# Optimization experiments

Measured on AMD Instinct MI355X. Metric: run time of the kernel, lower is better.

Reference implementation:

```python
import jax, jax.numpy as jnp
import numpy as np

N_NODES = 100000
N_EDGES = 1600000
N_REL = 8
N_HEADS = 4
IN_FEAT = 128
OUT_FEAT = 64
D_HEAD = OUT_FEAT // N_HEADS
LEAKY_SLOPE = 0.2


def setup_inputs() -> dict:
    key = jax.random.key(0)
    ks = jax.random.split(key, 8)
    inputs = jax.random.normal(ks[0], (N_NODES, IN_FEAT), dtype=jnp.float32)
    conv_weights = jax.random.normal(ks[1], (N_REL, N_HEADS, IN_FEAT, D_HEAD), dtype=jnp.float32) * (1.0 / np.sqrt(IN_FEAT))
    attn_l = jax.random.normal(ks[2], (N_REL, N_HEADS, D_HEAD), dtype=jnp.float32) * (1.0 / np.sqrt(D_HEAD))
    attn_r = jax.random.normal(ks[3], (N_REL, N_HEADS, D_HEAD), dtype=jnp.float32) * (1.0 / np.sqrt(D_HEAD))
    h_bias = jax.random.normal(ks[4], (OUT_FEAT,), dtype=jnp.float32)
    src_idx = jax.random.randint(ks[5], (N_EDGES,), 0, N_NODES, dtype=jnp.int64) if jax.config.jax_enable_x64 else jax.random.randint(ks[5], (N_EDGES,), 0, N_NODES, dtype=jnp.int32)
    dst_idx = jax.random.randint(ks[6], (N_EDGES,), 0, N_NODES, dtype=src_idx.dtype)
    rel_idx = jax.random.randint(ks[7], (N_EDGES,), 0, N_REL, dtype=src_idx.dtype)
    return {"inputs": inputs, "conv_weights": conv_weights, "attn_l": attn_l,
            "attn_r": attn_r, "h_bias": h_bias, "src_idx": src_idx,
            "dst_idx": dst_idx, "rel_idx": rel_idx}


def reference(inputs, conv_weights, attn_l, attn_r, h_bias, src_idx, dst_idx, rel_idx):
    N = inputs.shape[0]
    # Per-node per-relation projection: [N, R, H, Dh]
    # (equivalent math to the per-relation grouped matmul over unique nodes)
    proj = jnp.einsum('ni,rhid->nrhd', inputs, conv_weights)
    # Gather per-edge src/dst projected features under the edge's relation: [E, H, Dh]
    feat_src = proj[src_idx, rel_idx]
    feat_dst = proj[dst_idx, rel_idx]
    # Attention logits per edge/head: [E, H]
    el = jnp.sum(feat_src * attn_l[rel_idx], axis=-1)
    er = jnp.sum(feat_dst * attn_r[rel_idx], axis=-1)
    score = jax.nn.leaky_relu(el + er, negative_slope=LEAKY_SLOPE)
    # Edge softmax over incoming edges of each destination node (per head)
    smax = jax.ops.segment_max(score, dst_idx, num_segments=N)        # [N, H]
    e = jnp.exp(score - smax[dst_idx])                                # [E, H]
    denom = jax.ops.segment_sum(e, dst_idx, num_segments=N)          # [N, H]
    alpha = e / denom[dst_idx]                                        # [E, H]
    # Weighted aggregation of src features to dst nodes: [N, H, Dh]
    h = jax.ops.segment_sum(alpha[..., None] * feat_src, dst_idx, num_segments=N)
    h = h.reshape(N, OUT_FEAT) + h_bias
    return h
```

## Files before the change

kernel.cpp:

```cpp
#include <hip/hip_runtime.h>
#include <hip/hip_bf16.h>


#define NN 100000
#define NNP 100096
#define NE 1600000
#define NH 4
#define INF_ 128
#define DH 16
#define NCOL 576
#define LEAKY 0.2f
#define NBUCK 391
#define BSHIFT 8
#define CHUNK 4096
#define CAP 5120
#define WEXT_BLOCKS 288

typedef __hip_bfloat16 bf16;
typedef __attribute__((ext_vector_type(8))) short bf16x8;
typedef __attribute__((ext_vector_type(4))) short bf16x4;
typedef __attribute__((ext_vector_type(4))) float f32x4;

static __device__ __forceinline__ short f2bs(float x) {
    bf16 b = __float2bfloat16(x);
    return *reinterpret_cast<short*>(&b);
}
static __device__ __forceinline__ float bflo(unsigned u) { return __uint_as_float(u << 16); }
static __device__ __forceinline__ float bfhi(unsigned u) { return __uint_as_float(u & 0xffff0000u); }

__global__ __launch_bounds__(256) void wext_scatter(
    const float* __restrict__ W, const float* __restrict__ al, const float* __restrict__ ar,
    short* __restrict__ wxt2,
    const int* __restrict__ src, const int* __restrict__ dst, const int* __restrict__ rel,
    int* __restrict__ gCursor, int* __restrict__ pairbuf) {
    __shared__ int hist[NBUCK];
    int t = threadIdx.x;

    if (blockIdx.x >= WEXT_BLOCKS) {
        int blk = blockIdx.x - WEXT_BLOCKS;
        for (int i = t; i < NBUCK; i += 256) hist[i] = 0;
        __syncthreads();
        int base = blk * CHUNK;
        #pragma unroll
        for (int j = 0; j < CHUNK / 256; ++j) {
            int e = base + j * 256 + t;
            if (e < NE) atomicAdd(&hist[dst[e] >> BSHIFT], 1);
        }
        __syncthreads();
        for (int i = t; i < NBUCK; i += 256) {
            int v = hist[i];
            hist[i] = v ? (i * CAP + atomicAdd(&gCursor[i], v)) : 0;
        }
        __syncthreads();
        #pragma unroll
        for (int j = 0; j < CHUNK / 256; ++j) {
            int e = base + j * 256 + t;
            if (e < NE) {
                int d = dst[e];
                int b = d >> BSHIFT;
                int rec = ((d & 255) << 20) | (src[e] * 8 + rel[e]);
                int pos = atomicAdd(&hist[b], 1);
                pairbuf[pos] = rec;
            }
        }
        return;
    }

    int idx = blockIdx.x * 256 + t;
    int e = idx & 7, lane = (idx >> 3) & 63, ct = (idx >> 9) & 3, ks = (idx >> 11) & 3, cb = idx >> 13;
    int g = lane >> 4, r = lane & 15;
    int c = cb * 64 + ct * 16 + r;
    int k = ks * 32 + g * 8 + e;
    float v;
    if (c < 512) {
        int rr = c >> 6, rem = c & 63, h = rem >> 4, d = rem & 15;
        v = W[((rr * NH + h) * INF_ + k) * DH + d];
    } else {
        int rh = c - 512;
        const float* a = al;
        if (rh >= 32) { rh -= 32; a = ar; }
        int rr = rh >> 2, h = rh & 3;
        const float* wp = &W[((rr * NH + h) * INF_ + k) * DH];
        const float* ap = &a[(rr * NH + h) * DH];
        float s = 0.f;
        #pragma unroll
        for (int d = 0; d < DH; ++d) s += wp[d] * ap[d];
        v = s;
    }
    wxt2[idx] = f2bs(v);
}

__global__ __launch_bounds__(256) void gemm_direct(
    const float* __restrict__ A, const short* __restrict__ WxT2,
    bf16* __restrict__ projR, float* __restrict__ elr) {
    __shared__ short As[16384];
    __shared__ short Bs[8192];
    int t = threadIdx.x;
    int wv = t >> 6, lane = t & 63;
    int n0 = blockIdx.x * 128;
    int g = lane >> 4, r = lane & 15;

    #pragma unroll
    for (int j = 0; j < 8; ++j) {
        int i = j * 256 + t;
        int row = i >> 4, c8 = i & 15;
        int gr = n0 + row;
        bf16x8 v;
        if (gr < NN) {
            float4 f0 = *(const float4*)&A[gr * INF_ + c8 * 8];
            float4 f1 = *(const float4*)&A[gr * INF_ + c8 * 8 + 4];
            v[0] = f2bs(f0.x); v[1] = f2bs(f0.y); v[2] = f2bs(f0.z); v[3] = f2bs(f0.w);
            v[4] = f2bs(f1.x); v[5] = f2bs(f1.y); v[6] = f2bs(f1.z); v[7] = f2bs(f1.w);
        } else {
            v = (bf16x8)(short)0;
        }
        *(bf16x8*)&As[(row * 16 + (c8 ^ (row & 7))) * 8] = v;
    }
    bf16x8 breg[4];
    #pragma unroll
    for (int q = 0; q < 4; ++q)
        breg[q] = *(const bf16x8*)&WxT2[(q * 256 + t) * 8];
    __syncthreads();

    bf16x8 afr[2][4];
    #pragma unroll
    for (int nt = 0; nt < 2; ++nt) {
        int row = wv * 32 + nt * 16 + r;
        #pragma unroll
        for (int ks = 0; ks < 4; ++ks)
            afr[nt][ks] = *(const bf16x8*)&As[(row * 16 + ((ks * 4 + g) ^ (r & 7))) * 8];
    }
    __syncthreads();
    short* Csh = &As[wv * 4096];
    float* Csf = (float*)Csh;
    int n0w = n0 + wv * 32;

    for (int cb = 0; cb < 9; ++cb) {
        #pragma unroll
        for (int q = 0; q < 4; ++q)
            *(bf16x8*)&Bs[(q * 256 + t) * 8] = breg[q];
        __syncthreads();
        if (cb < 8) {
            #pragma unroll
            for (int q = 0; q < 4; ++q)
                breg[q] = *(const bf16x8*)&WxT2[((cb + 1) * 1024 + q * 256 + t) * 8];
        }

        f32x4 acc[2][4] = {};
        #pragma unroll
        for (int ks = 0; ks < 4; ++ks) {
            #pragma unroll
            for (int ct = 0; ct < 4; ++ct) {
                bf16x8 b = *(const bf16x8*)&Bs[((ks * 4 + ct) * 64 + lane) * 8];
                acc[0][ct] = __builtin_amdgcn_mfma_f32_16x16x32_bf16(b, afr[0][ks], acc[0][ct], 0, 0, 0);
                acc[1][ct] = __builtin_amdgcn_mfma_f32_16x16x32_bf16(b, afr[1][ks], acc[1][ct], 0, 0, 0);
            }
        }
        if (cb < 8) {
            #pragma unroll
            for (int nt = 0; nt < 2; ++nt) {
                int rr = nt * 16 + r;
                #pragma unroll
                for (int ct = 0; ct < 4; ++ct) {
                    bf16x4 p;
                    p[0] = f2bs(acc[nt][ct][0]); p[1] = f2bs(acc[nt][ct][1]);
                    p[2] = f2bs(acc[nt][ct][2]); p[3] = f2bs(acc[nt][ct][3]);
                    *(bf16x4*)&Csh[rr * 64 + (((ct * 4 + g) ^ ((rr & 7) << 1)) << 2)] = p;
                }
            }
            __builtin_amdgcn_wave_barrier();
            size_t base = ((size_t)cb * NN + n0w) * 64;
            #pragma unroll
            for (int q = 0; q < 4; ++q) {
                int rr = (lane >> 3) + q * 8;
                if (n0w + rr < NN) {
                    bf16x8 vv = *(const bf16x8*)&Csh[rr * 64 + (((lane & 7) ^ (rr & 7)) << 3)];
                    __builtin_nontemporal_store(vv, (bf16x8*)&((short*)projR)[base + q * 512 + lane * 8]);
                }
            }
            __builtin_amdgcn_wave_barrier();
        } else {
            #pragma unroll
            for (int nt = 0; nt < 2; ++nt) {
                int rr = nt * 16 + r;
                #pragma unroll
                for (int ct = 0; ct < 4; ++ct)
                    *(f32x4*)&Csf[rr * 64 + (((ct * 4 + g) ^ ((rr & 7) << 1)) << 2)] = acc[nt][ct];
            }
            __builtin_amdgcn_wave_barrier();
            #pragma unroll
            for (int q = 0; q < 8; ++q) {
                int rr = (lane >> 4) + q * 4;
                if (n0w + rr < NN) {
                    f32x4 vv = *(const f32x4*)&Csf[rr * 64 + (((lane & 15) ^ ((rr & 7) << 1)) << 2)];
                    __builtin_nontemporal_store(vv, (f32x4*)&elr[(size_t)n0w * 64 + q * 256 + lane * 4]);
                }
            }
        }
        __syncthreads();
    }
}

__global__ __launch_bounds__(256) void exact_place(
    const int* __restrict__ gCursor, const int* __restrict__ pairbuf,
    int2* __restrict__ offdeg, int2* __restrict__ rec2) {
    __shared__ int hist[256];
    __shared__ int tsum[256];
    int b = blockIdx.x, t = threadIdx.x;
    int start = b * CAP, cnt = gCursor[b];
    hist[t] = 0;
    __syncthreads();
    for (int i = t; i < cnt; i += 256) atomicAdd(&hist[pairbuf[start + i] >> 20], 1);
    __syncthreads();
    int own = hist[t];
    tsum[t] = own;
    __syncthreads();
    for (int st = 1; st < 256; st <<= 1) {
        int y = (t >= st) ? tsum[t - st] : 0;
        __syncthreads();
        tsum[t] += y;
        __syncthreads();
    }
    int excl = start + tsum[t] - own;
    int node = b * 256 + t;
    if (node < NN) offdeg[node] = make_int2(excl, own);
    __syncthreads();
    hist[t] = excl;
    __syncthreads();
    for (int i = t; i < cnt; i += 256) {
        int rec = pairbuf[start + i];
        int pos = atomicAdd(&hist[rec >> 20], 1);
        int sr = rec & 0xFFFFF;
        rec2[pos] = make_int2((sr >> 3) * 64 + (sr & 7) * 4,
                              (sr & 7) * (NN * 64) + (sr >> 3) * 64);
    }
}

__global__ __launch_bounds__(256) void agg(
    const int2* __restrict__ offdeg, const int2* __restrict__ rec2,
    const float* __restrict__ elr, const bf16* __restrict__ projR,
    const float* __restrict__ bias, float* __restrict__ out) {
    __shared__ float s_alpha[4][64][4];
    __shared__ int   s_pidx[4][64];
    __shared__ float s_er[4][32];
    int wv = threadIdx.x >> 6, lane = threadIdx.x & 63;
    int d = blockIdx.x * 4 + wv;
    if (d >= NN) return;
    int2 od = offdeg[d];
    int off = od.x, deg = od.y;
    int end = off + deg;

    if (lane < 32) s_er[wv][lane] = elr[d * 64 + 32 + lane];
    __builtin_amdgcn_wave_barrier();
    asm volatile("s_waitcnt lgkmcnt(0)" ::: "memory");

    if (deg == 0) {
        if (lane < 32) {
            float2 bb = *(const float2*)&bias[lane * 2];
            *(float2*)&out[d * 64 + lane * 2] = bb;
        }
    } else if (deg <= 64) {
        int i = off + lane;
        float e0 = 0.f, e1 = 0.f, e2 = 0.f, e3 = 0.f;
        int pidx = 0;
        if (i < end) {
            int2 rv = rec2[i];
            pidx = rv.y;
            float4 el4 = *(const float4*)&elr[rv.x];
            int erb = rv.x & 63;
            float x;
            x = el4.x + s_er[wv][erb + 0]; x = x > 0.f ? x : LEAKY * x; e0 = __expf(x);
            x = el4.y + s_er[wv][erb + 1]; x = x > 0.f ? x : LEAKY * x; e1 = __expf(x);
            x = el4.z + s_er[wv][erb + 2]; x = x > 0.f ? x : LEAKY * x; e2 = __expf(x);
            x = el4.w + s_er[wv][erb + 3]; x = x > 0.f ? x : LEAKY * x; e3 = __expf(x);
        }
        s_pidx[wv][lane] = pidx;
        *(float4*)&s_alpha[wv][lane][0] = make_float4(e0, e1, e2, e3);
        __builtin_amdgcn_wave_barrier();
        asm volatile("s_waitcnt lgkmcnt(0)" ::: "memory");

        int col2 = (lane & 31) * 2;
        int hl = lane >> 5;
        int h2 = (lane & 31) >> 3;
        float acc0 = 0.f, acc1 = 0.f, dsum = 0.f;
        int j = 0;
        for (; j + 8 <= deg; j += 8) {
            unsigned uu[4];
            #pragma unroll
            for (int p = 0; p < 4; ++p) {
                int myp = s_pidx[wv][j + 2 * p + hl];
                uu[p] = *(const unsigned*)&projR[myp + col2];
            }
            #pragma unroll
            for (int p = 0; p < 4; ++p) {
                float a_self = s_alpha[wv][j + 2 * p + hl][h2];
                float a_oth  = s_alpha[wv][j + 2 * p + 1 - hl][h2];
                unsigned uo = __shfl_xor((int)uu[p], 32);
                acc0 = fmaf(a_self, bflo(uu[p]), acc0);
                acc1 = fmaf(a_self, bfhi(uu[p]), acc1);
                acc0 = fmaf(a_oth, bflo(uo), acc0);
                acc1 = fmaf(a_oth, bfhi(uo), acc1);
                dsum += a_self + a_oth;
            }
        }
        for (; j + 2 <= deg; j += 2) {
            int myp = s_pidx[wv][j + hl];
            unsigned u = *(const unsigned*)&projR[myp + col2];
            float a_self = s_alpha[wv][j + hl][h2];
            float a_oth  = s_alpha[wv][j + 1 - hl][h2];
            unsigned uo = __shfl_xor((int)u, 32);
            acc0 = fmaf(a_self, bflo(u), acc0);
            acc1 = fmaf(a_self, bfhi(u), acc1);
            acc0 = fmaf(a_oth, bflo(uo), acc0);
            acc1 = fmaf(a_oth, bfhi(uo), acc1);
            dsum += a_self + a_oth;
        }
        if (j < deg) {
            int myp = s_pidx[wv][j];
            unsigned u = *(const unsigned*)&projR[myp + col2];
            float a = s_alpha[wv][j][h2];
            acc0 = fmaf(a, bflo(u), acc0);
            acc1 = fmaf(a, bfhi(u), acc1);
            dsum += a;
        }
        if (lane < 32) {
            float inv = 1.0f / dsum;
            float2 bb = *(const float2*)&bias[col2];
            float2 o;
            o.x = acc0 * inv + bb.x;
            o.y = acc1 * inv + bb.y;
            *(float2*)&out[d * 64 + col2] = o;
        }
    } else {
        int c = lane, h = c >> 4;
        float dsum0 = 0.f, dsum1 = 0.f, dsum2 = 0.f, dsum3 = 0.f;
        for (int i = off + lane; i < end; i += 64) {
            int2 rv = rec2[i];
            float4 el4 = *(const float4*)&elr[rv.x];
            int erb = rv.x & 63;
            float x;
            x = el4.x + s_er[wv][erb + 0]; x = x > 0.f ? x : LEAKY * x; dsum0 += __expf(x);
            x = el4.y + s_er[wv][erb + 1]; x = x > 0.f ? x : LEAKY * x; dsum1 += __expf(x);
            x = el4.z + s_er[wv][erb + 2]; x = x > 0.f ? x : LEAKY * x; dsum2 += __expf(x);
            x = el4.w + s_er[wv][erb + 3]; x = x > 0.f ? x : LEAKY * x; dsum3 += __expf(x);
        }
        #pragma unroll
        for (int m = 32; m; m >>= 1) {
            dsum0 += __shfl_xor(dsum0, m, 64);
            dsum1 += __shfl_xor(dsum1, m, 64);
            dsum2 += __shfl_xor(dsum2, m, 64);
            dsum3 += __shfl_xor(dsum3, m, 64);
        }
        float dh = (h == 0) ? dsum0 : (h == 1) ? dsum1 : (h == 2) ? dsum2 : dsum3;
        float rd = 1.0f / dh;
        float acc = 0.f;
        for (int i = off; i < end; ++i) {
            int2 rv = rec2[i];
            float x = elr[rv.x + h] + s_er[wv][(rv.x & 63) + h];
            x = x > 0.f ? x : LEAKY * x;
            acc = fmaf(__expf(x) * rd, __bfloat162float(projR[rv.y + c]), acc);
        }
        out[d * 64 + c] = acc + bias[c];
    }
}

extern "C" void kernel_launch(void* const* d_in, const int* in_sizes, int n_in,
                              void* d_out, int out_size, void* d_ws, size_t ws_size,
                              hipStream_t stream) {
    const float* inputs = (const float*)d_in[0];
    const float* convw  = (const float*)d_in[1];
    const float* attn_l = (const float*)d_in[2];
    const float* attn_r = (const float*)d_in[3];
    const float* h_bias = (const float*)d_in[4];
    const int*   src    = (const int*)d_in[5];
    const int*   dst    = (const int*)d_in[6];
    const int*   rel    = (const int*)d_in[7];
    float* out = (float*)d_out;

    char* ws = (char*)d_ws;
    size_t o = 0;
    bf16* projR = (bf16*)(ws + o);  o += 102400000ull;
    float* elr  = (float*)(ws + o); o += 25600000ull;
    short* wxt2 = (short*)(ws + o); o += 147456;
    int2* offdeg = (int2*)(ws + o); o += 800768;
    int* gCursor = (int*)(ws + o);  o += 2048;
    int* pairbuf = (int*)(ws + o);  o += (size_t)NBUCK * CAP * 4;
    int2* rec2   = (int2*)(ws + o); o += (size_t)NBUCK * CAP * 8;

    hipMemsetAsync(gCursor, 0, NBUCK * sizeof(int), stream);
    hipLaunchKernelGGL(wext_scatter, dim3(WEXT_BLOCKS + NBUCK), dim3(256), 0, stream,
                       convw, attn_l, attn_r, wxt2, src, dst, rel, gCursor, pairbuf);
    hipLaunchKernelGGL(gemm_direct, dim3(NNP / 128), dim3(256), 0, stream, inputs, wxt2, projR, elr);
    hipLaunchKernelGGL(exact_place, dim3(NBUCK), dim3(256), 0, stream, gCursor, pairbuf, offdeg, rec2);
    hipLaunchKernelGGL(agg, dim3(25000), dim3(256), 0, stream, offdeg, rec2, elr, projR, h_bias, out);
}
```

Measured before the change: 166.9 us.

## Move edge bucket scatter into GEMM kernel and use regular stores

The edge-bucketing scatter blocks move out of the weight-extension kernel and into the GEMM launch as leading blocks, reusing the GEMM's shared memory for the histogram. The latency-bound atomic scatter work can then run alongside the compute-bound projection GEMM instead of alongside the tiny weight-prep kernel. Nontemporal stores for projR and elr also become regular stores, which may leave those results in cache for the aggregation kernel. The cost is a larger, mixed-role launch whose two block types compete for the same CUs.

```diff
diff --git a/kernel.cpp b/kernel.cpp
--- a/kernel.cpp
+++ b/kernel.cpp
@@ -14,7 +14,7 @@
 #define BSHIFT 8
 #define CHUNK 4096
 #define CAP 5120
-#define WEXT_BLOCKS 288
+#define GEMM_NB 782
 
 typedef __hip_bfloat16 bf16;
 typedef __attribute__((ext_vector_type(8))) short bf16x8;
@@ -28,45 +28,10 @@
 static __device__ __forceinline__ float bflo(unsigned u) { return __uint_as_float(u << 16); }
 static __device__ __forceinline__ float bfhi(unsigned u) { return __uint_as_float(u & 0xffff0000u); }
 
-__global__ __launch_bounds__(256) void wext_scatter(
-    const float* __restrict__ W, const float* __restrict__ al, const float* __restrict__ ar,
-    short* __restrict__ wxt2,
-    const int* __restrict__ src, const int* __restrict__ dst, const int* __restrict__ rel,
-    int* __restrict__ gCursor, int* __restrict__ pairbuf) {
-    __shared__ int hist[NBUCK];
-    int t = threadIdx.x;
-
-    if (blockIdx.x >= WEXT_BLOCKS) {
-        int blk = blockIdx.x - WEXT_BLOCKS;
-        for (int i = t; i < NBUCK; i += 256) hist[i] = 0;
-        __syncthreads();
-        int base = blk * CHUNK;
-        #pragma unroll
-        for (int j = 0; j < CHUNK / 256; ++j) {
-            int e = base + j * 256 + t;
-            if (e < NE) atomicAdd(&hist[dst[e] >> BSHIFT], 1);
-        }
-        __syncthreads();
-        for (int i = t; i < NBUCK; i += 256) {
-            int v = hist[i];
-            hist[i] = v ? (i * CAP + atomicAdd(&gCursor[i], v)) : 0;
-        }
-        __syncthreads();
-        #pragma unroll
-        for (int j = 0; j < CHUNK / 256; ++j) {
-            int e = base + j * 256 + t;
-            if (e < NE) {
-                int d = dst[e];
-                int b = d >> BSHIFT;
-                int rec = ((d & 255) << 20) | (src[e] * 8 + rel[e]);
-                int pos = atomicAdd(&hist[b], 1);
-                pairbuf[pos] = rec;
-            }
-        }
-        return;
-    }
-
-    int idx = blockIdx.x * 256 + t;
+__global__ void wext(const float* __restrict__ W, const float* __restrict__ al,
+                     const float* __restrict__ ar, short* __restrict__ wxt2) {
+    int idx = blockIdx.x * 256 + threadIdx.x;
+    if (idx >= NCOL * INF_) return;
     int e = idx & 7, lane = (idx >> 3) & 63, ct = (idx >> 9) & 3, ks = (idx >> 11) & 3, cb = idx >> 13;
     int g = lane >> 4, r = lane & 15;
     int c = cb * 64 + ct * 16 + r;
@@ -90,14 +55,48 @@
     wxt2[idx] = f2bs(v);
 }
 
-__global__ __launch_bounds__(256) void gemm_direct(
+__global__ __launch_bounds__(256) void gemm_fused(
     const float* __restrict__ A, const short* __restrict__ WxT2,
-    bf16* __restrict__ projR, float* __restrict__ elr) {
+    bf16* __restrict__ projR, float* __restrict__ elr,
+    const int* __restrict__ src, const int* __restrict__ dst, const int* __restrict__ rel,
+    int* __restrict__ gCursor, int* __restrict__ pairbuf) {
     __shared__ short As[16384];
     __shared__ short Bs[8192];
     int t = threadIdx.x;
+
+    if (blockIdx.x < NBUCK) {
+        int* hist = (int*)As;
+        int blk = blockIdx.x;
+        for (int i = t; i < NBUCK; i += 256) hist[i] = 0;
+        __syncthreads();
+        int base = blk * CHUNK;
+        #pragma unroll
+        for (int j = 0; j < CHUNK / 256; ++j) {
+            int e = base + j * 256 + t;
+            if (e < NE) atomicAdd(&hist[dst[e] >> BSHIFT], 1);
+        }
+        __syncthreads();
+        for (int i = t; i < NBUCK; i += 256) {
+            int v = hist[i];
+            hist[i] = v ? (i * CAP + atomicAdd(&gCursor[i], v)) : 0;
+        }
+        __syncthreads();
+        #pragma unroll
+        for (int j = 0; j < CHUNK / 256; ++j) {
+            int e = base + j * 256 + t;
+            if (e < NE) {
+                int d = dst[e];
+                int b = d >> BSHIFT;
+                int rec = ((d & 255) << 20) | (src[e] * 8 + rel[e]);
+                int pos = atomicAdd(&hist[b], 1);
+                pairbuf[pos] = rec;
+            }
+        }
+        return;
+    }
+
     int wv = t >> 6, lane = t & 63;
-    int n0 = blockIdx.x * 128;
+    int n0 = (blockIdx.x - NBUCK) * 128;
     int g = lane >> 4, r = lane & 15;
 
     #pragma unroll
@@ -175,7 +174,7 @@
                 int rr = (lane >> 3) + q * 8;
                 if (n0w + rr < NN) {
                     bf16x8 vv = *(const bf16x8*)&Csh[rr * 64 + (((lane & 7) ^ (rr & 7)) << 3)];
-                    __builtin_nontemporal_store(vv, (bf16x8*)&((short*)projR)[base + q * 512 + lane * 8]);
+                    *(bf16x8*)&((short*)projR)[base + q * 512 + lane * 8] = vv;
                 }
             }
             __builtin_amdgcn_wave_barrier();
@@ -193,7 +192,7 @@
                 int rr = (lane >> 4) + q * 4;
                 if (n0w + rr < NN) {
                     f32x4 vv = *(const f32x4*)&Csf[rr * 64 + (((lane & 15) ^ ((rr & 7) << 1)) << 2)];
-                    __builtin_nontemporal_store(vv, (f32x4*)&elr[(size_t)n0w * 64 + q * 256 + lane * 4]);
+                    *(f32x4*)&elr[(size_t)n0w * 64 + q * 256 + lane * 4] = vv;
                 }
             }
         }
@@ -388,9 +387,9 @@
     int2* rec2   = (int2*)(ws + o); o += (size_t)NBUCK * CAP * 8;
 
     hipMemsetAsync(gCursor, 0, NBUCK * sizeof(int), stream);
-    hipLaunchKernelGGL(wext_scatter, dim3(WEXT_BLOCKS + NBUCK), dim3(256), 0, stream,
-                       convw, attn_l, attn_r, wxt2, src, dst, rel, gCursor, pairbuf);
-    hipLaunchKernelGGL(gemm_direct, dim3(NNP / 128), dim3(256), 0, stream, inputs, wxt2, projR, elr);
+    hipLaunchKernelGGL(wext, dim3(288), dim3(256), 0, stream, convw, attn_l, attn_r, wxt2);
+    hipLaunchKernelGGL(gemm_fused, dim3(NBUCK + GEMM_NB), dim3(256), 0, stream,
+                       inputs, wxt2, projR, elr, src, dst, rel, gCursor, pairbuf);
     hipLaunchKernelGGL(exact_place, dim3(NBUCK), dim3(256), 0, stream, gCursor, pairbuf, offdeg, rec2);
     hipLaunchKernelGGL(agg, dim3(25000), dim3(256), 0, stream, offdeg, rec2, elr, projR, h_bias, out);
 }
```

Result: faster. 158.7 us (-4.9%).
